# Optimization experiments

Hardware: AMD Instinct MI355X
Metric: run time of the kernel (lower is better)

## Reference

```python
import jax, jax.numpy as jnp
from jax import lax
import numpy as np

B, T, I, H, O = 128, 256, 256, 1024, 128


def _rnn_layer(x, W_ih, W_hh, b_ih, b_hh):
    # x: [B, T, D_in] -> hidden states [B, T, H]
    # precompute input projection for all timesteps (batched GEMM)
    xW = jnp.einsum('btd,hd->bth', x, W_ih) + b_ih + b_hh  # [B, T, H]

    def step(h, xw_t):
        h = jnp.tanh(xw_t + h @ W_hh.T)  # [B, H]
        return h, h

    h0 = jnp.zeros((x.shape[0], W_hh.shape[0]), x.dtype)
    _, hs = lax.scan(step, h0, jnp.swapaxes(xW, 0, 1))  # hs: [T, B, H]
    return jnp.swapaxes(hs, 0, 1)  # [B, T, H]


def setup_inputs() -> dict:
    key = jax.random.key(0)
    ks = jax.random.split(key, 11)
    s_ih0 = 1.0 / np.sqrt(H)
    inp = {
        'X': jax.random.normal(ks[0], (B, T, I), jnp.float32),
        'W_ih0': jax.random.uniform(ks[1], (H, I), jnp.float32, -s_ih0, s_ih0),
        'W_hh0': jax.random.uniform(ks[2], (H, H), jnp.float32, -s_ih0, s_ih0),
        'b_ih0': jax.random.uniform(ks[3], (H,), jnp.float32, -s_ih0, s_ih0),
        'b_hh0': jax.random.uniform(ks[4], (H,), jnp.float32, -s_ih0, s_ih0),
        'W_ih1': jax.random.uniform(ks[5], (H, H), jnp.float32, -s_ih0, s_ih0),
        'W_hh1': jax.random.uniform(ks[6], (H, H), jnp.float32, -s_ih0, s_ih0),
        'b_ih1': jax.random.uniform(ks[7], (H,), jnp.float32, -s_ih0, s_ih0),
        'b_hh1': jax.random.uniform(ks[8], (H,), jnp.float32, -s_ih0, s_ih0),
        'W_fc': jax.random.uniform(ks[9], (O, H), jnp.float32, -s_ih0, s_ih0),
        'b_fc': jax.random.uniform(ks[10], (O,), jnp.float32, -s_ih0, s_ih0),
    }
    return inp


def reference(X, W_ih0, W_hh0, b_ih0, b_hh0, W_ih1, W_hh1, b_ih1, b_hh1, W_fc, b_fc):
    h1 = _rnn_layer(X, W_ih0, W_hh0, b_ih0, b_hh0)   # layer 0: [B, T, H]
    h2 = _rnn_layer(h1, W_ih1, W_hh1, b_ih1, b_hh1)  # layer 1: [B, T, H]
    last = h2[:, -1, :]                               # [B, H]
    return last @ W_fc.T + b_fc                       # [B, O]
```

## Files before the change

### kernel.cpp

```cpp
#include <hip/hip_runtime.h>
#include <stdint.h>
#include <stddef.h>

#define B_ 128
#define T_ 256
#define I_ 256
#define H_ 1024
#define O_ 128

typedef __attribute__((ext_vector_type(8))) __bf16 bf16x8;
typedef __attribute__((ext_vector_type(4))) float f32x4;
typedef unsigned long long u64;



__global__ void split_kernel(const float* __restrict__ src, __bf16* __restrict__ hi,
                             __bf16* __restrict__ lo, int n) {
    int i = blockIdx.x * blockDim.x + threadIdx.x;
    int stride = gridDim.x * blockDim.x;
    for (; i < n; i += stride) {
        float v = src[i];
        __bf16 h = (__bf16)v;
        hi[i] = h;
        lo[i] = (__bf16)(v - (float)h);
    }
}

__global__ void pack_x(const float* __restrict__ X, __bf16* __restrict__ xh,
                       __bf16* __restrict__ xl) {
    int i = blockIdx.x * 256 + threadIdx.x;
    int lnidx = i & 15;
    int kg   = (i >> 4) & 31;
    int bgrp = (i >> 9) & 7;
    int t    = i >> 12;
    int b = bgrp * 16 + lnidx;
    const float* xs = X + (long)b * T_ * I_ + (long)t * I_ + kg * 8;
    float4 f0 = *(const float4*)xs;
    float4 f1 = *(const float4*)(xs + 4);
    float f[8] = {f0.x, f0.y, f0.z, f0.w, f1.x, f1.y, f1.z, f1.w};
    bf16x8 hv, lv;
    #pragma unroll
    for (int j = 0; j < 8; ++j) {
        __bf16 h = (__bf16)f[j];
        hv[j] = h;
        lv[j] = (__bf16)(f[j] - (float)h);
    }
    long o = (long)t * 32768 + (long)(bgrp * 32 + kg) * 128 + lnidx * 8;
    *(bf16x8*)(xh + o) = hv;
    *(bf16x8*)(xl + o) = lv;
}

__global__ void bias_sum_kernel(const float* __restrict__ a, const float* __restrict__ b,
                                float* __restrict__ o, int n) {
    int i = blockIdx.x * blockDim.x + threadIdx.x;
    if (i < n) o[i] = a[i] + b[i];
}

__global__ void transpose_fc(const float* __restrict__ w, float* __restrict__ wt) {
    int i = blockIdx.x * blockDim.x + threadIdx.x;
    if (i < O_ * H_) {
        int o = i / H_, k = i - o * H_;
        wt[k * O_ + o] = w[i];
    }
}


__device__ __forceinline__ void wave_wait(unsigned* bar, int slot, unsigned v) {
    while (__hip_atomic_load(&bar[slot * 64 + 32], __ATOMIC_RELAXED,
                             __HIP_MEMORY_SCOPE_AGENT) < v)
        __builtin_amdgcn_s_sleep(1);
    asm volatile("" ::: "memory");
}

__device__ __forceinline__ void bar_arrive(unsigned* bar, int slot, unsigned k) {
    asm volatile("s_waitcnt vmcnt(0)" ::: "memory");
    __syncthreads();
    if (threadIdx.x == 0) {
        unsigned old = __hip_atomic_fetch_add(&bar[slot * 64], 1u, __ATOMIC_RELAXED,
                                              __HIP_MEMORY_SCOPE_AGENT);
        if (old == k * 32u + 31u)
            __hip_atomic_store(&bar[slot * 64 + 32], k + 1u, __ATOMIC_RELAXED,
                               __HIP_MEMORY_SCOPE_AGENT);
    }
}

union Frag { u64 d[2]; bf16x8 v; };

template <int CPW, int SEG0CH, bool CACHED0>
__device__ __forceinline__ void step_full(
    const __bf16* __restrict__ A0h, const __bf16* __restrict__ A0l,
    const __bf16* __restrict__ Sh,  const __bf16* __restrict__ Sl,
    const bf16x8 (&wh)[CPW][2], const bf16x8 (&wl)[CPW][2],
    const float* __restrict__ bs,
    __bf16* __restrict__ Soh, __bf16* __restrict__ Sol,
    int bt, int jt, int w, float* red,
    unsigned* bar, int ldSlot, unsigned ldVal,
    int epSlotA, unsigned epValA, int epSlotB, unsigned epValB)
{
    const int lane = threadIdx.x & 63;
    const int ln = lane & 15;
    const int q  = lane >> 4;

    wave_wait(bar, ldSlot, ldVal);

    f32x4 acc[2][2][2];
    #pragma unroll
    for (int s = 0; s < 2; ++s)
        #pragma unroll
        for (int n = 0; n < 2; ++n)
            #pragma unroll
            for (int r = 0; r < 2; ++r)
                acc[s][n][r] = (f32x4){0.f, 0.f, 0.f, 0.f};

    constexpr int PF = 4;
    Frag SH[PF][2], SL[PF][2];

    auto issue = [&](int c, Frag (&FH)[2], Frag (&FL)[2]) {
        const int gC = w * CPW + c;
        if (gC < SEG0CH) {
            #pragma unroll
            for (int s = 0; s < 2; ++s) {
                long off = ((long)(bt * 2 + s) * (SEG0CH * 4) + gC * 4 + q) * 128 + ln * 8;
                if constexpr (CACHED0) {
                    FH[s].v = *(const bf16x8*)(A0h + off);
                    FL[s].v = *(const bf16x8*)(A0l + off);
                } else {
                    const u64* ph = (const u64*)(A0h + off);
                    const u64* pl = (const u64*)(A0l + off);
                    FH[s].d[0] = __hip_atomic_load(ph,     __ATOMIC_RELAXED, __HIP_MEMORY_SCOPE_AGENT);
                    FH[s].d[1] = __hip_atomic_load(ph + 1, __ATOMIC_RELAXED, __HIP_MEMORY_SCOPE_AGENT);
                    FL[s].d[0] = __hip_atomic_load(pl,     __ATOMIC_RELAXED, __HIP_MEMORY_SCOPE_AGENT);
                    FL[s].d[1] = __hip_atomic_load(pl + 1, __ATOMIC_RELAXED, __HIP_MEMORY_SCOPE_AGENT);
                }
            }
        } else {
            #pragma unroll
            for (int s = 0; s < 2; ++s) {
                long off = ((long)(bt * 2 + s) * 128 + (gC - SEG0CH) * 4 + q) * 128 + ln * 8;
                const u64* ph = (const u64*)(Sh + off);
                const u64* pl = (const u64*)(Sl + off);
                FH[s].d[0] = __hip_atomic_load(ph,     __ATOMIC_RELAXED, __HIP_MEMORY_SCOPE_AGENT);
                FH[s].d[1] = __hip_atomic_load(ph + 1, __ATOMIC_RELAXED, __HIP_MEMORY_SCOPE_AGENT);
                FL[s].d[0] = __hip_atomic_load(pl,     __ATOMIC_RELAXED, __HIP_MEMORY_SCOPE_AGENT);
                FL[s].d[1] = __hip_atomic_load(pl + 1, __ATOMIC_RELAXED, __HIP_MEMORY_SCOPE_AGENT);
            }
        }
    };

    #pragma unroll
    for (int i = 0; i < PF; ++i)
        if (i < CPW) issue(i, SH[i], SL[i]);

    #pragma unroll
    for (int c = 0; c < CPW; ++c) {
        bf16x8 ah[2], al[2];
        #pragma unroll
        for (int s = 0; s < 2; ++s) { ah[s] = SH[c & (PF - 1)][s].v; al[s] = SL[c & (PF - 1)][s].v; }
        if (c + PF < CPW) issue(c + PF, SH[c & (PF - 1)], SL[c & (PF - 1)]);
        #pragma unroll
        for (int s = 0; s < 2; ++s)
            #pragma unroll
            for (int n = 0; n < 2; ++n) {
                acc[s][n][0] = __builtin_amdgcn_mfma_f32_16x16x32_bf16(ah[s], wh[c][n], acc[s][n][0], 0, 0, 0);
                acc[s][n][1] = __builtin_amdgcn_mfma_f32_16x16x32_bf16(al[s], wh[c][n], acc[s][n][1], 0, 0, 0);
                acc[s][n][1] = __builtin_amdgcn_mfma_f32_16x16x32_bf16(ah[s], wl[c][n], acc[s][n][1], 0, 0, 0);
            }
    }

    {
        float* my = red + w * 1088;
        #pragma unroll
        for (int s = 0; s < 2; ++s)
            #pragma unroll
            for (int n = 0; n < 2; ++n) {
                f32x4 sum = acc[s][n][0] + acc[s][n][1];
                #pragma unroll
                for (int r = 0; r < 4; ++r)
                    my[(s * 16 + q * 4 + r) * 34 + n * 16 + ln] = sum[r];
            }
    }
    __syncthreads();

    wave_wait(bar, epSlotA, epValA);
    wave_wait(bar, epSlotB, epValB);

    {
        int tid = threadIdx.x;
        int row = tid >> 4;
        int jp  = tid & 15;
        int c0 = jp * 2;
        float v0 = 0.f, v1 = 0.f;
        #pragma unroll
        for (int w8 = 0; w8 < 8; ++w8) {
            float2 v = *(const float2*)&red[w8 * 1088 + row * 34 + c0];
            v0 += v.x;
            v1 += v.y;
        }
        int j0 = jt * 32 + c0;
        float h0 = tanhf(v0 + bs[j0]);
        float h1v = tanhf(v1 + bs[j0 + 1]);
        union { __bf16 b; unsigned short u; } x0h, x0l, x1h, x1l;
        x0h.b = (__bf16)h0;  x0l.b = (__bf16)(h0 - (float)x0h.b);
        x1h.b = (__bf16)h1v; x1l.b = (__bf16)(h1v - (float)x1h.b);
        unsigned uh = (unsigned)x0h.u | ((unsigned)x1h.u << 16);
        unsigned ul = (unsigned)x0l.u | ((unsigned)x1l.u << 16);
        long idx = ((long)(bt * 2 + (row >> 4)) * 128 + jt * 4 + (c0 >> 3)) * 128
                 + (row & 15) * 8 + (c0 & 7);
        __hip_atomic_store((unsigned*)(Soh + idx), uh, __ATOMIC_RELAXED, __HIP_MEMORY_SCOPE_AGENT);
        __hip_atomic_store((unsigned*)(Sol + idx), ul, __ATOMIC_RELAXED, __HIP_MEMORY_SCOPE_AGENT);
    }
}

struct PArgs {
    const __bf16 *xh, *xl;
    const __bf16 *Wi0h, *Wi0l, *Wr0h, *Wr0l;
    const __bf16 *Wi1h, *Wi1l, *Wr1h, *Wr1l;
    const float *bs0, *bs1;
    __bf16 *s0ah, *s0al, *s0bh, *s0bl;
    __bf16 *s1ah, *s1al, *s1bh, *s1bl;
    unsigned* bar;
};

__global__ __launch_bounds__(512, 2) void persistent_rnn(PArgs a) {
    __shared__ float red[8 * 1088];
    const int w = threadIdx.x >> 6;
    const int lane = threadIdx.x & 63;
    const int ln = lane & 15;
    const int q  = lane >> 4;
    const int layer = blockIdx.x >> 7;
    const int r7 = blockIdx.x & 127;
    const int jt = r7 & 31;
    const int bt = r7 >> 5;
    const int slotL0 = 0 * 4 + bt;
    const int slotL1 = 1 * 4 + bt;

    if (layer == 0) {
        bf16x8 wh[5][2], wl[5][2];
        #pragma unroll
        for (int c = 0; c < 5; ++c) {
            int gC = w * 5 + c;
            #pragma unroll
            for (int n = 0; n < 2; ++n) {
                int jr = jt * 32 + n * 16 + ln;
                if (gC < 8) {
                    wh[c][n] = *(const bf16x8*)(a.Wi0h + (long)jr * 256 + gC * 32 + q * 8);
                    wl[c][n] = *(const bf16x8*)(a.Wi0l + (long)jr * 256 + gC * 32 + q * 8);
                } else {
                    wh[c][n] = *(const bf16x8*)(a.Wr0h + (long)jr * 1024 + (gC - 8) * 32 + q * 8);
                    wl[c][n] = *(const bf16x8*)(a.Wr0l + (long)jr * 1024 + (gC - 8) * 32 + q * 8);
                }
            }
        }
        for (int t = 0; t < T_; ++t) {
            const __bf16* sinh_ = (t & 1) ? a.s0bh : a.s0ah;
            const __bf16* sinl_ = (t & 1) ? a.s0bl : a.s0al;
            __bf16* south      = (t & 1) ? a.s0ah : a.s0bh;
            __bf16* soutl      = (t & 1) ? a.s0al : a.s0bl;
            unsigned ldVal = (w >= 1) ? (unsigned)t : 0u;
            step_full<5, 8, true>(a.xh + (long)t * 32768, a.xl + (long)t * 32768,
                                  sinh_, sinl_, wh, wl, a.bs0,
                                  south, soutl, bt, jt, w, red,
                                  a.bar, slotL0, ldVal,
                                  slotL0, (w == 0) ? (unsigned)t : 0u,
                                  slotL1, (t >= 1) ? (unsigned)(t - 1) : 0u);
            bar_arrive(a.bar, slotL0, (unsigned)t);
        }
    } else {
        bf16x8 wh[8][2], wl[8][2];
        #pragma unroll
        for (int c = 0; c < 8; ++c) {
            int gC = w * 8 + c;
            #pragma unroll
            for (int n = 0; n < 2; ++n) {
                int jr = jt * 32 + n * 16 + ln;
                if (gC < 32) {
                    wh[c][n] = *(const bf16x8*)(a.Wi1h + (long)jr * 1024 + gC * 32 + q * 8);
                    wl[c][n] = *(const bf16x8*)(a.Wi1l + (long)jr * 1024 + gC * 32 + q * 8);
                } else {
                    wh[c][n] = *(const bf16x8*)(a.Wr1h + (long)jr * 1024 + (gC - 32) * 32 + q * 8);
                    wl[c][n] = *(const bf16x8*)(a.Wr1l + (long)jr * 1024 + (gC - 32) * 32 + q * 8);
                }
            }
        }
        for (int r = 1; r <= T_; ++r) {
            int t1 = r - 1;
            const __bf16* h1h = (t1 & 1) ? a.s0ah : a.s0bh;
            const __bf16* h1l = (t1 & 1) ? a.s0al : a.s0bl;
            const __bf16* sinh_ = (t1 & 1) ? a.s1bh : a.s1ah;
            const __bf16* sinl_ = (t1 & 1) ? a.s1bl : a.s1al;
            __bf16* south       = (t1 & 1) ? a.s1ah : a.s1bh;
            __bf16* soutl       = (t1 & 1) ? a.s1al : a.s1bl;
            int ldSlot       = (w < 4) ? slotL0 : slotL1;
            unsigned ldVal   = (w < 4) ? (unsigned)r
                                       : ((r >= 2) ? (unsigned)(r - 1) : 0u);
            step_full<8, 32, false>(h1h, h1l, sinh_, sinl_, wh, wl, a.bs1,
                                    south, soutl, bt, jt, w, red,
                                    a.bar, ldSlot, ldVal,
                                    slotL1, (r >= 2) ? (unsigned)(r - 1) : 0u,
                                    slotL1, 0u);
            bar_arrive(a.bar, slotL1, (unsigned)(r - 1));
        }
    }
}

__global__ __launch_bounds__(128) void fc_kernel(const __bf16* __restrict__ sph,
                                                 const __bf16* __restrict__ spl,
                                                 const float* __restrict__ wt,
                                                 const float* __restrict__ bfc,
                                                 float* __restrict__ out) {
    int b = blockIdx.x;
    int o = threadIdx.x;
    float acc = 0.f;
    #pragma unroll 2
    for (int kg = 0; kg < 128; ++kg) {
        long off = ((long)(b >> 4) * 128 + kg) * 128 + (b & 15) * 8;
        bf16x8 hv = *(const bf16x8*)(sph + off);
        bf16x8 lv = *(const bf16x8*)(spl + off);
        #pragma unroll
        for (int j = 0; j < 8; ++j) {
            float x = (float)hv[j] + (float)lv[j];
            acc += x * wt[(kg * 8 + j) * O_ + o];
        }
    }
    out[b * O_ + o] = acc + bfc[o];
}


extern "C" void kernel_launch(void* const* d_in, const int* in_sizes, int n_in,
                              void* d_out, int out_size, void* d_ws, size_t ws_size,
                              hipStream_t stream) {
    const float* X     = (const float*)d_in[0];
    const float* Wih0  = (const float*)d_in[1];
    const float* Whh0  = (const float*)d_in[2];
    const float* bih0  = (const float*)d_in[3];
    const float* bhh0  = (const float*)d_in[4];
    const float* Wih1  = (const float*)d_in[5];
    const float* Whh1  = (const float*)d_in[6];
    const float* bih1  = (const float*)d_in[7];
    const float* bhh1  = (const float*)d_in[8];
    const float* Wfc   = (const float*)d_in[9];
    const float* bfc   = (const float*)d_in[10];
    float* out = (float*)d_out;

    char* p = (char*)d_ws;
    auto alloc = [&](size_t bytes) -> void* {
        void* r = (void*)p;
        p += (bytes + 255) & ~(size_t)255;
        return r;
    };
    const size_t nW0 = (size_t)H_ * I_;
    const size_t nW  = (size_t)H_ * H_;
    const size_t planeSt = (size_t)131072;
    __bf16* xh   = (__bf16*)alloc((size_t)T_ * 32768 * 2);
    __bf16* xl   = (__bf16*)alloc((size_t)T_ * 32768 * 2);
    __bf16* W0h  = (__bf16*)alloc(nW0 * 2);
    __bf16* W0l  = (__bf16*)alloc(nW0 * 2);
    __bf16* Wh0h = (__bf16*)alloc(nW * 2);
    __bf16* Wh0l = (__bf16*)alloc(nW * 2);
    __bf16* Wi1h = (__bf16*)alloc(nW * 2);
    __bf16* Wi1l = (__bf16*)alloc(nW * 2);
    __bf16* Wh1h = (__bf16*)alloc(nW * 2);
    __bf16* Wh1l = (__bf16*)alloc(nW * 2);
    __bf16* s0ah = (__bf16*)alloc(planeSt * 2);
    __bf16* s0al = (__bf16*)alloc(planeSt * 2);
    __bf16* s0bh = (__bf16*)alloc(planeSt * 2);
    __bf16* s0bl = (__bf16*)alloc(planeSt * 2);
    __bf16* s1ah = (__bf16*)alloc(planeSt * 2);
    __bf16* s1al = (__bf16*)alloc(planeSt * 2);
    __bf16* s1bh = (__bf16*)alloc(planeSt * 2);
    __bf16* s1bl = (__bf16*)alloc(planeSt * 2);
    float* wfct = (float*)alloc((size_t)H_ * O_ * 4);
    float* bs0  = (float*)alloc((size_t)H_ * 4);
    float* bs1  = (float*)alloc((size_t)H_ * 4);
    unsigned* bar = (unsigned*)alloc(4096);
    (void)ws_size; (void)n_in; (void)in_sizes; (void)out_size;

    pack_x<<<4096, 256, 0, stream>>>(X, xh, xl);
    split_kernel<<<512, 256, 0, stream>>>(Wih0, W0h, W0l, (int)nW0);
    split_kernel<<<1024, 256, 0, stream>>>(Whh0, Wh0h, Wh0l, (int)nW);
    split_kernel<<<1024, 256, 0, stream>>>(Wih1, Wi1h, Wi1l, (int)nW);
    split_kernel<<<1024, 256, 0, stream>>>(Whh1, Wh1h, Wh1l, (int)nW);
    bias_sum_kernel<<<4, 256, 0, stream>>>(bih0, bhh0, bs0, H_);
    bias_sum_kernel<<<4, 256, 0, stream>>>(bih1, bhh1, bs1, H_);
    transpose_fc<<<(O_ * H_ + 255) / 256, 256, 0, stream>>>(Wfc, wfct);

    hipMemsetAsync(s0ah, 0, planeSt * 2, stream);
    hipMemsetAsync(s0al, 0, planeSt * 2, stream);
    hipMemsetAsync(s1ah, 0, planeSt * 2, stream);
    hipMemsetAsync(s1al, 0, planeSt * 2, stream);
    hipMemsetAsync(bar, 0, 4096, stream);

    PArgs args;
    args.xh = xh; args.xl = xl;
    args.Wi0h = W0h; args.Wi0l = W0l; args.Wr0h = Wh0h; args.Wr0l = Wh0l;
    args.Wi1h = Wi1h; args.Wi1l = Wi1l; args.Wr1h = Wh1h; args.Wr1l = Wh1l;
    args.bs0 = bs0; args.bs1 = bs1;
    args.s0ah = s0ah; args.s0al = s0al; args.s0bh = s0bh; args.s0bl = s0bl;
    args.s1ah = s1ah; args.s1al = s1al; args.s1bh = s1bh; args.s1bl = s1bl;
    args.bar = bar;
    void* kp[] = { &args };
    hipLaunchCooperativeKernel((void*)persistent_rnn, dim3(256), dim3(512), kp, 0, stream);

    fc_kernel<<<B_, O_, 0, stream>>>(s1ah, s1al, wfct, bfc, out);
}
```

Baseline: 2.267 ms.

## Replace counter barriers with per-block flags and fine-grained dependency waits

Each block now publishes its own progress flag with a plain atomic store instead of incrementing a shared counter, which removes atomic contention on one address. Waiters poll the flag array one lane per producer and check all of them at once with a wave vote. Each wave waits only on the producer blocks whose hidden-state columns it actually reads, so it can start before the whole group has finished. The cost is more memory traffic while polling, and the index arithmetic for the partial waits is fragile.

After: 2.778 ms. 22.5% more time.

```diff
diff --git a/kernel.cpp b/kernel.cpp
--- a/kernel.cpp
+++ b/kernel.cpp
@@ -65,23 +65,23 @@
 }
 
 
-__device__ __forceinline__ void wave_wait(unsigned* bar, int slot, unsigned v) {
-    while (__hip_atomic_load(&bar[slot * 64 + 32], __ATOMIC_RELAXED,
-                             __HIP_MEMORY_SCOPE_AGENT) < v)
-        __builtin_amdgcn_s_sleep(1);
+__device__ __forceinline__ void flags_wait(const unsigned* f, int n, unsigned v) {
+    if (n == 0) return;
+    int lane = threadIdx.x & 63;
+    const unsigned* p = f + ((lane < n) ? lane : 0);
+    for (;;) {
+        unsigned x = __hip_atomic_load(p, __ATOMIC_RELAXED, __HIP_MEMORY_SCOPE_AGENT);
+        if (__all((int)(x >= v))) break;
+        __builtin_amdgcn_s_sleep(2);
+    }
     asm volatile("" ::: "memory");
 }
 
-__device__ __forceinline__ void bar_arrive(unsigned* bar, int slot, unsigned k) {
+__device__ __forceinline__ void post_flag(unsigned* f, unsigned v) {
     asm volatile("s_waitcnt vmcnt(0)" ::: "memory");
     __syncthreads();
-    if (threadIdx.x == 0) {
-        unsigned old = __hip_atomic_fetch_add(&bar[slot * 64], 1u, __ATOMIC_RELAXED,
-                                              __HIP_MEMORY_SCOPE_AGENT);
-        if (old == k * 32u + 31u)
-            __hip_atomic_store(&bar[slot * 64 + 32], k + 1u, __ATOMIC_RELAXED,
-                               __HIP_MEMORY_SCOPE_AGENT);
-    }
+    if (threadIdx.x == 0)
+        __hip_atomic_store(f, v, __ATOMIC_RELAXED, __HIP_MEMORY_SCOPE_AGENT);
 }
 
 union Frag { u64 d[2]; bf16x8 v; };
@@ -94,14 +94,15 @@
     const float* __restrict__ bs,
     __bf16* __restrict__ Soh, __bf16* __restrict__ Sol,
     int bt, int jt, int w, float* red,
-    unsigned* bar, int ldSlot, unsigned ldVal,
-    int epSlotA, unsigned epValA, int epSlotB, unsigned epValB)
+    const unsigned* ldF, int ldN, unsigned ldV,
+    const unsigned* gAF, unsigned gAV,
+    const unsigned* gBF, unsigned gBV)
 {
     const int lane = threadIdx.x & 63;
     const int ln = lane & 15;
     const int q  = lane >> 4;
 
-    wave_wait(bar, ldSlot, ldVal);
+    flags_wait(ldF, ldN, ldV);
 
     f32x4 acc[2][2][2];
     #pragma unroll
@@ -181,8 +182,8 @@
     }
     __syncthreads();
 
-    wave_wait(bar, epSlotA, epValA);
-    wave_wait(bar, epSlotB, epValB);
+    flags_wait(gAF, 32, gAV);
+    if (gBF) flags_wait(gBF, 32, gBV);
 
     {
         int tid = threadIdx.x;
@@ -231,8 +232,8 @@
     const int r7 = blockIdx.x & 127;
     const int jt = r7 & 31;
     const int bt = r7 >> 5;
-    const int slotL0 = 0 * 4 + bt;
-    const int slotL1 = 1 * 4 + bt;
+    unsigned* fL0 = a.bar + bt * 64;
+    unsigned* fL1 = a.bar + 512 + bt * 64;
 
     if (layer == 0) {
         bf16x8 wh[5][2], wl[5][2];
@@ -251,19 +252,20 @@
                 }
             }
         }
+        const int pLo = (w * 5 >= 8) ? (w * 5 - 8) : 0;
+        const int ldN = (w == 0) ? 0 : (w * 5 - 4 - pLo + 1);
         for (int t = 0; t < T_; ++t) {
             const __bf16* sinh_ = (t & 1) ? a.s0bh : a.s0ah;
             const __bf16* sinl_ = (t & 1) ? a.s0bl : a.s0al;
             __bf16* south      = (t & 1) ? a.s0ah : a.s0bh;
             __bf16* soutl      = (t & 1) ? a.s0al : a.s0bl;
-            unsigned ldVal = (w >= 1) ? (unsigned)t : 0u;
             step_full<5, 8, true>(a.xh + (long)t * 32768, a.xl + (long)t * 32768,
                                   sinh_, sinl_, wh, wl, a.bs0,
                                   south, soutl, bt, jt, w, red,
-                                  a.bar, slotL0, ldVal,
-                                  slotL0, (w == 0) ? (unsigned)t : 0u,
-                                  slotL1, (t >= 1) ? (unsigned)(t - 1) : 0u);
-            bar_arrive(a.bar, slotL0, (unsigned)t);
+                                  fL0 + pLo, ldN, (unsigned)t,
+                                  fL0, (unsigned)t,
+                                  fL1, (t >= 1) ? (unsigned)(t - 1) : 0u);
+            post_flag(&fL0[jt], (unsigned)(t + 1));
         }
     } else {
         bf16x8 wh[8][2], wl[8][2];
@@ -282,6 +284,7 @@
                 }
             }
         }
+        const unsigned* ldF = (w < 4) ? (fL0 + w * 8) : (fL1 + (w - 4) * 8);
         for (int r = 1; r <= T_; ++r) {
             int t1 = r - 1;
             const __bf16* h1h = (t1 & 1) ? a.s0ah : a.s0bh;
@@ -290,15 +293,13 @@
             const __bf16* sinl_ = (t1 & 1) ? a.s1bl : a.s1al;
             __bf16* south       = (t1 & 1) ? a.s1ah : a.s1bh;
             __bf16* soutl       = (t1 & 1) ? a.s1al : a.s1bl;
-            int ldSlot       = (w < 4) ? slotL0 : slotL1;
-            unsigned ldVal   = (w < 4) ? (unsigned)r
-                                       : ((r >= 2) ? (unsigned)(r - 1) : 0u);
+            unsigned ldV = (w < 4) ? (unsigned)r : (unsigned)(r - 1);
             step_full<8, 32, false>(h1h, h1l, sinh_, sinl_, wh, wl, a.bs1,
                                     south, soutl, bt, jt, w, red,
-                                    a.bar, ldSlot, ldVal,
-                                    slotL1, (r >= 2) ? (unsigned)(r - 1) : 0u,
-                                    slotL1, 0u);
-            bar_arrive(a.bar, slotL1, (unsigned)(r - 1));
+                                    ldF, 8, ldV,
+                                    fL1, (unsigned)(r - 1),
+                                    (const unsigned*)nullptr, 0u);
+            post_flag(&fL1[jt], (unsigned)r);
         }
     }
 }
```

## Replace per-wave spin waits with single-thread wait plus acquire fence

Applied to the files above, without the earlier changes.

Moves barrier polling from every wave to thread 0 of each block, followed by an agent-scope acquire fence and __syncthreads. Because of the fence, cross-block state loads can become ordinary vector loads instead of relaxed 64-bit atomic loads. The trade is that per-wave early starts are lost: layer-1 waves reading only the previous layer's output, and layer-0 waves reading x, now wait for every dependency before starting. It also adds an extra block-wide sync per step.

Measured after the change: 2.364 ms. 4.3% more time.

```diff
diff --git a/kernel.cpp b/kernel.cpp
--- a/kernel.cpp
+++ b/kernel.cpp
@@ -65,10 +65,20 @@
 }
 
 
-__device__ __forceinline__ void wave_wait(unsigned* bar, int slot, unsigned v) {
-    while (__hip_atomic_load(&bar[slot * 64 + 32], __ATOMIC_RELAXED,
-                             __HIP_MEMORY_SCOPE_AGENT) < v)
-        __builtin_amdgcn_s_sleep(1);
+__device__ __forceinline__ void deps_fence_wait(unsigned* bar, int sA, unsigned vA,
+                                                int sB, unsigned vB) {
+    if (threadIdx.x == 0) {
+        while (__hip_atomic_load(&bar[sA * 64 + 32], __ATOMIC_RELAXED,
+                                 __HIP_MEMORY_SCOPE_AGENT) < vA)
+            __builtin_amdgcn_s_sleep(2);
+        if (sB >= 0) {
+            while (__hip_atomic_load(&bar[sB * 64 + 32], __ATOMIC_RELAXED,
+                                     __HIP_MEMORY_SCOPE_AGENT) < vB)
+                __builtin_amdgcn_s_sleep(2);
+        }
+        __builtin_amdgcn_fence(__ATOMIC_ACQUIRE, "agent");
+    }
+    __syncthreads();
     asm volatile("" ::: "memory");
 }
 
@@ -86,7 +96,7 @@
 
 union Frag { u64 d[2]; bf16x8 v; };
 
-template <int CPW, int SEG0CH, bool CACHED0>
+template <int CPW, int SEG0CH>
 __device__ __forceinline__ void step_full(
     const __bf16* __restrict__ A0h, const __bf16* __restrict__ A0l,
     const __bf16* __restrict__ Sh,  const __bf16* __restrict__ Sl,
@@ -94,15 +104,12 @@
     const float* __restrict__ bs,
     __bf16* __restrict__ Soh, __bf16* __restrict__ Sol,
     int bt, int jt, int w, float* red,
-    unsigned* bar, int ldSlot, unsigned ldVal,
-    int epSlotA, unsigned epValA, int epSlotB, unsigned epValB)
+    unsigned* bar, int gSlot, unsigned gVal)
 {
     const int lane = threadIdx.x & 63;
     const int ln = lane & 15;
     const int q  = lane >> 4;
 
-    wave_wait(bar, ldSlot, ldVal);
-
     f32x4 acc[2][2][2];
     #pragma unroll
     for (int s = 0; s < 2; ++s)
@@ -121,28 +128,15 @@
             #pragma unroll
             for (int s = 0; s < 2; ++s) {
                 long off = ((long)(bt * 2 + s) * (SEG0CH * 4) + gC * 4 + q) * 128 + ln * 8;
-                if constexpr (CACHED0) {
-                    FH[s].v = *(const bf16x8*)(A0h + off);
-                    FL[s].v = *(const bf16x8*)(A0l + off);
-                } else {
-                    const u64* ph = (const u64*)(A0h + off);
-                    const u64* pl = (const u64*)(A0l + off);
-                    FH[s].d[0] = __hip_atomic_load(ph,     __ATOMIC_RELAXED, __HIP_MEMORY_SCOPE_AGENT);
-                    FH[s].d[1] = __hip_atomic_load(ph + 1, __ATOMIC_RELAXED, __HIP_MEMORY_SCOPE_AGENT);
-                    FL[s].d[0] = __hip_atomic_load(pl,     __ATOMIC_RELAXED, __HIP_MEMORY_SCOPE_AGENT);
-                    FL[s].d[1] = __hip_atomic_load(pl + 1, __ATOMIC_RELAXED, __HIP_MEMORY_SCOPE_AGENT);
-                }
+                FH[s].v = *(const bf16x8*)(A0h + off);
+                FL[s].v = *(const bf16x8*)(A0l + off);
             }
         } else {
             #pragma unroll
             for (int s = 0; s < 2; ++s) {
                 long off = ((long)(bt * 2 + s) * 128 + (gC - SEG0CH) * 4 + q) * 128 + ln * 8;
-                const u64* ph = (const u64*)(Sh + off);
-                const u64* pl = (const u64*)(Sl + off);
-                FH[s].d[0] = __hip_atomic_load(ph,     __ATOMIC_RELAXED, __HIP_MEMORY_SCOPE_AGENT);
-                FH[s].d[1] = __hip_atomic_load(ph + 1, __ATOMIC_RELAXED, __HIP_MEMORY_SCOPE_AGENT);
-                FL[s].d[0] = __hip_atomic_load(pl,     __ATOMIC_RELAXED, __HIP_MEMORY_SCOPE_AGENT);
-                FL[s].d[1] = __hip_atomic_load(pl + 1, __ATOMIC_RELAXED, __HIP_MEMORY_SCOPE_AGENT);
+                FH[s].v = *(const bf16x8*)(Sh + off);
+                FL[s].v = *(const bf16x8*)(Sl + off);
             }
         }
     };
@@ -181,8 +175,14 @@
     }
     __syncthreads();
 
-    wave_wait(bar, epSlotA, epValA);
-    wave_wait(bar, epSlotB, epValB);
+    if (gSlot >= 0) {
+        if (threadIdx.x == 0) {
+            while (__hip_atomic_load(&bar[gSlot * 64 + 32], __ATOMIC_RELAXED,
+                                     __HIP_MEMORY_SCOPE_AGENT) < gVal)
+                __builtin_amdgcn_s_sleep(2);
+        }
+        __syncthreads();
+    }
 
     {
         int tid = threadIdx.x;
@@ -256,13 +256,11 @@
             const __bf16* sinl_ = (t & 1) ? a.s0bl : a.s0al;
             __bf16* south      = (t & 1) ? a.s0ah : a.s0bh;
             __bf16* soutl      = (t & 1) ? a.s0al : a.s0bl;
-            unsigned ldVal = (w >= 1) ? (unsigned)t : 0u;
-            step_full<5, 8, true>(a.xh + (long)t * 32768, a.xl + (long)t * 32768,
-                                  sinh_, sinl_, wh, wl, a.bs0,
-                                  south, soutl, bt, jt, w, red,
-                                  a.bar, slotL0, ldVal,
-                                  slotL0, (w == 0) ? (unsigned)t : 0u,
-                                  slotL1, (t >= 1) ? (unsigned)(t - 1) : 0u);
+            deps_fence_wait(a.bar, slotL0, (unsigned)t, -1, 0u);
+            step_full<5, 8>(a.xh + (long)t * 32768, a.xl + (long)t * 32768,
+                            sinh_, sinl_, wh, wl, a.bs0,
+                            south, soutl, bt, jt, w, red,
+                            a.bar, slotL1, (t >= 1) ? (unsigned)(t - 1) : 0u);
             bar_arrive(a.bar, slotL0, (unsigned)t);
         }
     } else {
@@ -290,14 +288,11 @@
             const __bf16* sinl_ = (t1 & 1) ? a.s1bl : a.s1al;
             __bf16* south       = (t1 & 1) ? a.s1ah : a.s1bh;
             __bf16* soutl       = (t1 & 1) ? a.s1al : a.s1bl;
-            int ldSlot       = (w < 4) ? slotL0 : slotL1;
-            unsigned ldVal   = (w < 4) ? (unsigned)r
-                                       : ((r >= 2) ? (unsigned)(r - 1) : 0u);
-            step_full<8, 32, false>(h1h, h1l, sinh_, sinl_, wh, wl, a.bs1,
-                                    south, soutl, bt, jt, w, red,
-                                    a.bar, ldSlot, ldVal,
-                                    slotL1, (r >= 2) ? (unsigned)(r - 1) : 0u,
-                                    slotL1, 0u);
+            deps_fence_wait(a.bar, slotL0, (unsigned)r,
+                            slotL1, (r >= 2) ? (unsigned)(r - 1) : 0u);
+            step_full<8, 32>(h1h, h1l, sinh_, sinl_, wh, wl, a.bs1,
+                             south, soutl, bt, jt, w, red,
+                             a.bar, -1, 0u);
             bar_arrive(a.bar, slotL1, (unsigned)(r - 1));
         }
     }
```
